# Kernel tuning notes

Hardware: AMD Instinct MI355X
Metric: run time of the kernel (lower is better)

The kernel has to match this reference:

```python
import jax, jax.numpy as jnp
import numpy as np


def conv2d(x, w, b, pad):
    # NCHW conv, stride 1, symmetric padding
    out = jax.lax.conv_general_dilated(
        x, w, window_strides=(1, 1), padding=[(pad, pad), (pad, pad)],
        dimension_numbers=("NCHW", "OIHW", "NCHW"))
    return out + b[None, :, None, None]


def setup_inputs() -> dict:
    key = jax.random.key(0)
    ks = jax.random.split(key, 18)
    B, C, H, W = 4, 256, 64, 64
    Cq = C // 16  # 16
    Ck = C // 8   # 32
    s = 0.02
    return {
        "x": jax.random.normal(ks[0], (B, C, H, W), jnp.float32),
        "dw1_w": jax.random.normal(ks[1], (Cq, C, 7, 7), jnp.float32) * s,
        "dw1_b": jnp.zeros((Cq,), jnp.float32),
        "dw2_w": jax.random.normal(ks[2], (Cq, C, 11, 11), jnp.float32) * s,
        "dw2_b": jnp.zeros((Cq,), jnp.float32),
        "key_w": jax.random.normal(ks[3], (Ck, C, 1, 1), jnp.float32) * s,
        "key_b": jnp.zeros((Ck,), jnp.float32),
        "value_w": jax.random.normal(ks[4], (C, C, 1, 1), jnp.float32) * s,
        "value_b": jnp.zeros((C,), jnp.float32),
        "conv1_w": jax.random.normal(ks[5], (Cq, C, 3, 3), jnp.float32) * s,
        "conv1_b": jnp.zeros((Cq,), jnp.float32),
        "conv2_w": jax.random.normal(ks[6], (C, Cq, 3, 3), jnp.float32) * s,
        "conv2_b": jnp.zeros((C,), jnp.float32),
        "se_w": jax.random.normal(ks[7], (C, C, 1, 1), jnp.float32) * s,
        "se_b": jnp.zeros((C,), jnp.float32),
        "gamma1": jnp.zeros((1,), jnp.float32) + 0.1,  # nonzero so attention path is exercised
        "gamma2": jnp.zeros((1,), jnp.float32) + 0.1,
    }


def reference(x, dw1_w, dw1_b, dw2_w, dw2_b, key_w, key_b, value_w, value_b,
              conv1_w, conv1_b, conv2_w, conv2_b, se_w, se_b, gamma1, gamma2):
    B, C, H, W = x.shape
    HW = H * W
    # q: concat of 7x7 and 11x11 conv branches -> (B, HW, C//8)
    q = jnp.concatenate([conv2d(x, dw1_w, dw1_b, 3), conv2d(x, dw2_w, dw2_b, 5)], axis=1)
    q = q.reshape(B, -1, HW).transpose(0, 2, 1)
    # k: 1x1 conv -> (B, C//8, HW)
    k = conv2d(x, key_w, key_b, 0).reshape(B, -1, HW)
    # raw (unscaled) full spatial attention, softmax over last dim
    att = jax.nn.softmax(jnp.einsum("bnc,bcm->bnm", q, k), axis=-1)  # (B, HW, HW)
    v = conv2d(x, value_w, value_b, 0).reshape(B, C, HW)
    out = jnp.einsum("bcm,bnm->bcn", v, att).reshape(B, C, H, W)
    # local conv branch + channel attention (SE)
    y = conv2d(jax.nn.silu(conv2d(x, conv1_w, conv1_b, 1)), conv2_w, conv2_b, 1)
    pooled = jnp.mean(y, axis=(2, 3), keepdims=True)  # (B, C, 1, 1)
    se = y * jax.nn.sigmoid(conv2d(pooled, se_w, se_b, 0))
    return gamma1 * out + gamma2 * se + x
```

## Files before the change

kernel.cpp:

```cpp
#include <hip/hip_runtime.h>

typedef unsigned short u16;
typedef unsigned u32;
typedef __bf16 bf16x8 __attribute__((ext_vector_type(8)));
typedef float f32x4 __attribute__((ext_vector_type(4)));
typedef float f32x16 __attribute__((ext_vector_type(16)));

#define MFMA16(A,B,C) __builtin_amdgcn_mfma_f32_16x16x32_bf16((A),(B),(C),0,0,0)
#define MFMA32(A,B,C) __builtin_amdgcn_mfma_f32_32x32x16_bf16((A),(B),(C),0,0,0)

__device__ __forceinline__ u16 f2b(float f){
  union { float f; unsigned u; } X; X.f = f;
  unsigned r = X.u + 0x7FFFu + ((X.u >> 16) & 1u);
  return (u16)(r >> 16);
}
__device__ __forceinline__ float b2f(u16 h){
  union { unsigned u; float f; } X; X.u = ((unsigned)h) << 16; return X.f;
}
__device__ __forceinline__ bf16x8 ld_frag(const u16* p){
  union { uint4 u; bf16x8 v; } U; U.u = *(const uint4*)p; return U.v;
}
__device__ __forceinline__ u32 pkbf(float a, float b){
  u32 r; asm("v_cvt_pk_bf16_f32 %0, %1, %2" : "=v"(r) : "v"(a), "v"(b)); return r;
}
__device__ __forceinline__ void pl32swap(u32& x, u32& y){
  auto r = __builtin_amdgcn_permlane32_swap(x, y, false, false);
  x = r[0]; y = r[1];
}
__device__ __forceinline__ void gld16(const u16* g, u16* l){
  __builtin_amdgcn_global_load_lds(
      (const __attribute__((address_space(1))) u32*)g,
      (__attribute__((address_space(3))) u32*)l, 16, 0, 0);
}

__device__ __forceinline__ void prep_w_body(int i,
    const float* __restrict__ dw1, const float* __restrict__ dw2,
    const float* __restrict__ cw1, const float* __restrict__ kw,
    const float* __restrict__ vw,  const float* __restrict__ cw2,
    u16* __restrict__ wB, u16* __restrict__ wC,
    u16* __restrict__ kwt, u16* __restrict__ vwt, u16* __restrict__ w2t,
    float* __restrict__ pooled){
  const int NB = 991232, NC = 73728, NK = 8192, NV = 65536, N2 = 40960;
  if(i < NB){
    int tap = i >> 13, rem = i & 8191;
    int chunk = rem >> 9, r2 = rem & 511;
    int oc = r2 >> 4, ci = chunk*16 + (r2 & 15);
    int dy = tap / 11, dx = tap - dy*11;
    float v;
    if(oc < 16){
      v = (dy >= 2 && dy <= 8 && dx >= 2 && dx <= 8) ? dw1[(oc*256 + ci)*49 + (dy-2)*7 + (dx-2)] : 0.f;
    } else {
      v = dw2[((oc-16)*256 + ci)*121 + tap];
    }
    wB[i] = f2b(v);
    return;
  }
  i -= NB;
  if(i < NC){
    int tap = i >> 13, rem = i & 8191;
    int chunk = rem >> 9, r2 = rem & 511;
    int oc = r2 >> 4, ci = chunk*16 + (r2 & 15);
    wC[i] = (oc < 16) ? f2b(cw1[(oc*256 + ci)*9 + tap]) : (u16)0;
    return;
  }
  i -= NC;
  if(i < NK){ kwt[i] = f2b(kw[i]); return; }
  i -= NK;
  if(i < NV){ vwt[i] = f2b(vw[i]); return; }
  i -= NV;
  if(i < N2){
    int co = i/160, kk = i - co*160;
    int tap = kk >> 4, ci = kk & 15;
    w2t[i] = (tap < 9) ? f2b(cw2[co*144 + ci*9 + tap]) : (u16)0;
    return;
  }
  i -= N2;
  if(i < 1024){ pooled[i] = 0.f; return; }
}

__device__ __forceinline__ void prep_x_body(int bid, int t, float* tile ,
    const float* __restrict__ x, u16* __restrict__ xp){
  const int b = bid >> 10, rem = bid & 1023;
  const int c0 = (rem >> 7) << 5, m0 = (rem & 127) << 5;
  { const int cg = t >> 5, mm = t & 31;
    #pragma unroll
    for(int i=0;i<4;i++)
      tile[(cg*4+i)*33 + mm] = x[((size_t)(b*256 + c0 + cg*4 + i) << 12) + m0 + mm];
  }
  __syncthreads();
  { const int cp = (t & 15) << 1, mloc = t >> 4;
    #pragma unroll
    for(int half = 0; half < 2; ++half){
      const int ml = half*16 + mloc;
      const int m = m0 + ml;
      const int yy = (m >> 6) + 5, xx = (m & 63) + 5;
      const int ci = c0 + cp;
      const int chunk = ci >> 4, wi = ci & 15;
      u16 lo = f2b(tile[cp*33 + ml]), hi = f2b(tile[(cp+1)*33 + ml]);
      *(unsigned*)&xp[(((size_t)(b*16 + chunk)*74 + yy)*80 + xx)*16 + wi] = ((unsigned)hi << 16) | lo;
    }
  }
}

__global__ __launch_bounds__(256) void k_prep(
    const float* __restrict__ x, u16* __restrict__ xp,
    const float* __restrict__ dw1, const float* __restrict__ dw2,
    const float* __restrict__ cw1, const float* __restrict__ kw,
    const float* __restrict__ vw,  const float* __restrict__ cw2,
    u16* __restrict__ wB, u16* __restrict__ wC,
    u16* __restrict__ kwt, u16* __restrict__ vwt, u16* __restrict__ w2t,
    float* __restrict__ pooled){
  __shared__ float tile[32*33];
  const int bid = blockIdx.x;
  if(bid < 4096){
    prep_x_body(bid, threadIdx.x, tile, x, xp);
  } else {
    prep_w_body((bid - 4096)*256 + threadIdx.x, dw1, dw2, cw1, kw, vw, cw2, wB, wC, kwt, vwt, w2t, pooled);
  }
}

__device__ __forceinline__ void qconv_body(int bid, int t, u16* buf ,
    const u16* __restrict__ xp, const u16* __restrict__ wB, const u16* __restrict__ wC,
    u16* __restrict__ qp){
  const int rg = bid & 15, b = (bid >> 4) & 3, kq = bid >> 6;
  const int y0 = rg << 2;
  const int wv = t >> 6, lane = t & 63;
  const int m = lane & 31, kh = lane >> 5;
  const int laneoff = m*16 + kh*8;
  const f32x16 z16 = {0.f,0.f,0.f,0.f,0.f,0.f,0.f,0.f,0.f,0.f,0.f,0.f,0.f,0.f,0.f,0.f};
  f32x16 accA = z16, accB = z16, acc1A = z16, acc1B = z16;

  #pragma unroll 1
  for(int c = 0; c < 2; ++c){
    const int chunk = kq*2 + c;
    const uint4* src = (const uint4*)(xp + ((size_t)((b*16 + chunk)*74 + y0))*1280);
    __syncthreads();
    for(int e = t; e < 2240; e += 256){
      ((uint4*)buf)[(e & 1)*1120 + (e >> 1)] = src[e];
    }
    __syncthreads();
    const u16* wBc = wB + chunk*512 + laneoff;
    const u16* wCc = wC + chunk*512 + laneoff;
    const u16* ap = buf + kh*8960 + (wv*80 + m)*8;
    bf16x8 Brow[2][11];
    #pragma unroll
    for(int dx = 0; dx < 11; ++dx) Brow[0][dx] = ld_frag(wBc + dx*8192);
    #pragma unroll
    for(int dy = 0; dy < 11; ++dy){
      if(dy < 10){
        const u16* wnext = wBc + (dy+1)*11*8192;
        #pragma unroll
        for(int dx = 0; dx < 11; ++dx) Brow[(dy+1)&1][dx] = ld_frag(wnext + dx*8192);
      }
      const u16* rowp = ap + dy*640;
      #pragma unroll
      for(int dx = 0; dx < 11; ++dx){
        bf16x8 B = Brow[dy&1][dx];
        bf16x8 A0 = ld_frag(rowp + dx*8);
        bf16x8 A1 = ld_frag(rowp + dx*8 + 256);
        accA = MFMA32(A0, B, accA);
        accB = MFMA32(A1, B, accB);
        if(dy >= 4 && dy <= 6 && dx >= 4 && dx <= 6){
          bf16x8 B1 = ld_frag(wCc + ((dy-4)*3 + (dx-4))*8192);
          acc1A = MFMA32(A0, B1, acc1A);
          acc1B = MFMA32(A1, B1, acc1B);
        }
      }
    }
  }

  u16* qb = qp + ((size_t)kq*16384 + (b << 12) + (y0 + wv)*64) * 48;
  #pragma unroll
  for(int reg = 0; reg < 16; ++reg){
    const int row = (reg & 3) + ((reg >> 2) << 3) + (kh << 2);
    qb[row*48 + m] = f2b(accA[reg]);
    qb[(32 + row)*48 + m] = f2b(accB[reg]);
    if(m < 16){
      qb[row*48 + 32 + m] = f2b(acc1A[reg]);
      qb[(32 + row)*48 + 32 + m] = f2b(acc1B[reg]);
    }
  }
}

__device__ __forceinline__ void kv_body(int bid, int tid,
    const u16* __restrict__ xp, const u16* __restrict__ vwt, const u16* __restrict__ kwt,
    const float* __restrict__ vb, const float* __restrict__ kb,
    u16* __restrict__ vt, u16* __restrict__ k_t){
  const int h = bid & 3, blk = (bid >> 2) & 63, b = bid >> 8;
  const int wv = tid >> 6, lane = tid & 63;
  const int col = lane & 15, quad = lane >> 4;
  const int m0 = (blk << 6) + (wv << 4);
  f32x4 z = {0.f,0.f,0.f,0.f};
  f32x4 av[4], ak[2];
  #pragma unroll
  for(int i=0;i<4;i++) av[i] = z;
  ak[0] = z; ak[1] = z;
  const int m = m0 + col;
  const int py = (m >> 6) + 5, pxx = (m & 63) + 5;
  #pragma unroll 1
  for(int ch = 0; ch < 8; ++ch){
    const int cio = ch*32 + quad*8;
    const int chunk = cio >> 4, wi = cio & 15;
    bf16x8 xf = ld_frag(xp + (((size_t)(b*16 + chunk)*74 + py)*80 + pxx)*16 + wi);
    #pragma unroll
    for(int ct2 = 0; ct2 < 4; ++ct2){
      bf16x8 wf = ld_frag(vwt + (((h*4 + ct2)*16 + col) << 8) + cio);
      av[ct2] = MFMA16(wf, xf, av[ct2]);
    }
    if(h == 0){
      #pragma unroll
      for(int kt = 0; kt < 2; ++kt){
        bf16x8 kf = ld_frag(kwt + ((kt*16 + col) << 8) + cio);
        ak[kt] = MFMA16(xf, kf, ak[kt]);
      }
    }
  }
  const size_t kgb = ((size_t)(b*256 + (m0 >> 4)));
  const int hi2 = col >> 3, j = col & 7;
  #pragma unroll
  for(int ct2 = 0; ct2 < 4; ++ct2){
    #pragma unroll
    for(int r = 0; r < 4; ++r){
      const int c = (h*4 + ct2)*16 + quad*4 + r;
      vt[((((kgb*8 + (c >> 5))*2 + hi2)*32) + (c & 31))*8 + j] = f2b(av[ct2][r] + vb[c]);
    }
  }
  if(h == 0){
    #pragma unroll
    for(int kt = 0; kt < 2; ++kt){
      #pragma unroll
      for(int r = 0; r < 4; ++r){
        const int mq = b*4096 + m0 + quad*4 + r;
        k_t[mq*32 + kt*16 + col] = f2b((ak[kt][r] + kb[kt*16 + col]) );
      }
    }
  }
}

__global__ __launch_bounds__(256, 2) void k_qconv_kv(
    const u16* __restrict__ xp, const u16* __restrict__ wB, const u16* __restrict__ wC,
    u16* __restrict__ qp,
    const u16* __restrict__ vwt, const u16* __restrict__ kwt,
    const float* __restrict__ vb, const float* __restrict__ kb,
    u16* __restrict__ vt, u16* __restrict__ k_t){
  __shared__ __align__(16) u16 buf[17920];
  const int bid = blockIdx.x;
  if(bid < 512) qconv_body(bid, threadIdx.x, buf, xp, wB, wC, qp);
  else          kv_body(bid - 512, threadIdx.x, xp, vwt, kwt, vb, kb, vt, k_t);
}

__global__ __launch_bounds__(256) void k_qfin(
    const u16* __restrict__ qp, const float* __restrict__ b7,
    const float* __restrict__ b11, const float* __restrict__ b1,
    u16* __restrict__ q_t, u16* __restrict__ t1){
  const int t = threadIdx.x, wv = t >> 6, lane = t & 63;
  const int px = blockIdx.x*4 + wv;
  if(lane >= 48) return;
  const size_t off = (size_t)px*48 + lane;
  float s = 0.f;
  #pragma unroll
  for(int sp = 0; sp < 8; ++sp) s += b2f(qp[off + (size_t)sp*786432]);
  const float LOG2E = 1.44269504f;
  if(lane < 16){
    q_t[px*32 + lane] = f2b((s + b7[lane]) * LOG2E);
  } else if(lane < 32){
    q_t[px*32 + lane] = f2b((s + b11[lane - 16]) * LOG2E);
  } else {
    float v = s + b1[lane - 32];
    t1[px*16 + lane - 32] = f2b(v / (1.f + __expf(-v)));
  }
}

__device__ __forceinline__ void attn_body(int bid, int t, u16* Vs ,
    const u16* __restrict__ q_t, const u16* __restrict__ k_t,
    const u16* __restrict__ vt, u16* __restrict__ Op,
    float* __restrict__ lsav){
  const int q0 = (bid & 31) << 7, b = (bid >> 5) & 3, ks = bid >> 7;
  const int wv = t >> 6, lane = t & 63;
  const int cq = lane & 31, hi = lane >> 5;

  const u16* qrow = q_t + ((size_t)(b*4096 + q0 + wv*32 + cq) << 5) + hi*8;
  const bf16x8 qf0 = ld_frag(qrow), qf1 = ld_frag(qrow + 16);
  const u16* kbase = k_t + ((size_t)(b*4096 + ks*1024 + cq) << 5) + hi*8;
  const u16* vsrc = vt + ((size_t)(b*256 + ks*64) << 12);

  const f32x16 z16 = {0.f,0.f,0.f,0.f,0.f,0.f,0.f,0.f,0.f,0.f,0.f,0.f,0.f,0.f,0.f,0.f};
  f32x16 acc[8];
  #pragma unroll
  for(int i=0;i<8;i++) acc[i] = z16;
  float lp0=0.f, lp1=0.f, lp2=0.f, lp3=0.f;

  #pragma unroll
  for(int s = 0; s < 8; ++s)
    gld16(vsrc + (size_t)(s*256 + t)*8, Vs + (s*256 + (wv << 6))*8);
  __builtin_amdgcn_sched_barrier(0);
  bf16x8 kc0 = ld_frag(kbase),        kc1 = ld_frag(kbase + 16);
  bf16x8 kc2 = ld_frag(kbase + 1024), kc3 = ld_frag(kbase + 1040);

  #pragma unroll 1
  for(int it = 0; it < 16; ++it){
    const int cur = it & 1;
    asm volatile("s_waitcnt vmcnt(4)" ::: "memory");
    __builtin_amdgcn_s_barrier();
    __builtin_amdgcn_sched_barrier(0);
    const bf16x8 ka0 = kc0, ka1 = kc1, ka2 = kc2, ka3 = kc3;
    if(it < 15){
      const u16* gb = vsrc + ((size_t)(it + 1) << 14);
      #pragma unroll
      for(int s = 0; s < 8; ++s)
        gld16(gb + (size_t)(s*256 + t)*8, Vs + (cur ^ 1)*16384 + (s*256 + (wv << 6))*8);
      __builtin_amdgcn_sched_barrier(0);
      const u16* kpn = kbase + ((size_t)(it + 1) << 11);
      kc0 = ld_frag(kpn);        kc1 = ld_frag(kpn + 16);
      kc2 = ld_frag(kpn + 1024); kc3 = ld_frag(kpn + 1040);
    }
    const u16* Vb = Vs + cur*16384 + hi*256 + cq*8;
    #pragma unroll
    for(int sub = 0; sub < 2; ++sub){
      const bf16x8 kf0 = sub ? ka2 : ka0;
      const bf16x8 kf1 = sub ? ka3 : ka1;
      f32x16 S = MFMA32(kf0, qf0, z16);
      S = MFMA32(kf1, qf1, S);
      float p[16];
      #pragma unroll
      for(int rr = 0; rr < 16; ++rr) p[rr] = exp2f(S[rr]);
      #pragma unroll
      for(int rr = 0; rr < 16; rr += 4){
        lp0 += p[rr]; lp1 += p[rr+1]; lp2 += p[rr+2]; lp3 += p[rr+3];
      }
      u32 a0 = pkbf(p[0], p[1]),   b0 = pkbf(p[4], p[5]);
      u32 a1 = pkbf(p[2], p[3]),   b1 = pkbf(p[6], p[7]);
      u32 c0 = pkbf(p[8], p[9]),   d0 = pkbf(p[12], p[13]);
      u32 c1 = pkbf(p[10], p[11]), d1 = pkbf(p[14], p[15]);
      pl32swap(a0, b0); pl32swap(a1, b1); pl32swap(c0, d0); pl32swap(c1, d1);
      union { u32 w[4]; bf16x8 v; } A0, A1;
      A0.w[0] = a0; A0.w[1] = a1; A0.w[2] = b0; A0.w[3] = b1;
      A1.w[0] = c0; A1.w[1] = c1; A1.w[2] = d0; A1.w[3] = d1;
      const u16* f0 = Vb + sub*8192;
      #pragma unroll
      for(int ct = 0; ct < 8; ++ct){
        acc[ct] = MFMA32(A0.v, ld_frag(f0 + ct*512),        acc[ct]);
        acc[ct] = MFMA32(A1.v, ld_frag(f0 + 4096 + ct*512), acc[ct]);
      }
    }
  }

  float lt = lp0 + lp1 + lp2 + lp3;
  lt += __shfl_xor(lt, 32);
  if(lane < 32)
    lsav[ks*16384 + b*4096 + q0 + wv*32 + cq] = lt;
  const float invl = 1.f / lt;
  u16* ob = Op + (((size_t)(ks*16384 + b*4096 + q0 + wv*32)) << 8) + cq;
  #pragma unroll
  for(int reg = 0; reg < 16; ++reg){
    const int row = (reg & 3) + ((reg >> 2) << 3) + (hi << 2);
    const float inv = __shfl(invl, row);
    u16* orow = ob + ((size_t)row << 8);
    #pragma unroll
    for(int ct = 0; ct < 8; ++ct)
      orow[ct*32] = f2b(acc[ct][reg] * inv);
  }
}

__device__ __forceinline__ void conv2_body(int bid, int t, u16* im_s , float* pool_s ,
    const u16* __restrict__ t1, const u16* __restrict__ w2t, const float* __restrict__ b2,
    u16* __restrict__ y_t, float* __restrict__ pooled){
  const int h = bid & 3, y = (bid >> 2) & 63, b = bid >> 8;
  if(t < 64) pool_s[t] = 0.f;
  const u16* t1b = t1 + ((size_t)(b*4096) << 4);
  { const int px = t >> 2, ci0 = (t & 3) << 2;
    #pragma unroll
    for(int tap = 0; tap < 9; ++tap){
      const int ky = (tap*11) >> 5, kx = tap - ky*3;
      const int ryy = y + ky - 1, rxx = px + kx - 1;
      uint2 val = make_uint2(0u, 0u);
      if((unsigned)ryy < 64u && (unsigned)rxx < 64u)
        val = *(const uint2*)(t1b + (((ryy << 6) + rxx) << 4) + ci0);
      *(uint2*)(im_s + px*168 + tap*16 + ci0) = val;
    }
    for(int e = t; e < 1024; e += 256){ im_s[(e >> 4)*168 + 144 + (e & 15)] = 0; }
  }
  __syncthreads();
  const int wv = t >> 6, lane = t & 63, col = lane & 15, quad = lane >> 4;
  const f32x4 z = {0.f,0.f,0.f,0.f};
  f32x4 acc[4];
  #pragma unroll
  for(int i=0;i<4;i++) acc[i] = z;
  #pragma unroll
  for(int ch = 0; ch < 5; ++ch){
    bf16x8 af = ld_frag(im_s + (wv*16 + col)*168 + ch*32 + quad*8);
    #pragma unroll
    for(int j = 0; j < 4; ++j){
      bf16x8 wf = ld_frag(w2t + ((h*4 + j)*16 + col)*160 + ch*32 + quad*8);
      acc[j] = MFMA16(af, wf, acc[j]);
    }
  }
  const int m0 = (y << 6) + (wv << 4) + (quad << 2);
  #pragma unroll
  for(int j = 0; j < 4; ++j){
    const int c = (h*4 + j)*16 + col;
    const float bias = b2[c];
    float s = 0.f;
    #pragma unroll
    for(int r = 0; r < 4; ++r){
      float v = acc[j][r] + bias;
      y_t[((size_t)(b*4096 + m0 + r) << 8) + c] = f2b(v);
      s += v;
    }
    s += __shfl_xor(s, 16); s += __shfl_xor(s, 32);
    if(quad == 0) atomicAdd(&pool_s[c - h*64], s);
  }
  __syncthreads();
  if(t < 64) atomicAdd(&pooled[b*256 + h*64 + t], pool_s[t]);
}

__global__ __launch_bounds__(256, 2) void k_attn_conv2(
    const u16* __restrict__ q_t, const u16* __restrict__ k_t,
    const u16* __restrict__ vt, u16* __restrict__ Op, float* __restrict__ lsav,
    const u16* __restrict__ t1, const u16* __restrict__ w2t, const float* __restrict__ b2,
    u16* __restrict__ y_t, float* __restrict__ pooled){
  __shared__ __align__(16) u16 shm[32768];
  const int bid = blockIdx.x;
  if(bid < 512) attn_body(bid, threadIdx.x, shm, q_t, k_t, vt, Op, lsav);
  else          conv2_body(bid - 512, threadIdx.x, shm, (float*)(shm + 10752), t1, w2t, b2, y_t, pooled);
}

__global__ __launch_bounds__(256) void k_final(
    const u16* __restrict__ Op, const u16* __restrict__ y_t, const float* __restrict__ x,
    const float* __restrict__ lsav, const float* __restrict__ pooled,
    const float* __restrict__ sew, const float* __restrict__ seb,
    const float* __restrict__ g1p, const float* __restrict__ g2p,
    float* __restrict__ out){
  __shared__ float tO[32][65];
  __shared__ float tY[32][65];
  __shared__ float gate_l[32];
  const int bid = blockIdx.x;
  const int b = bid >> 9, rem = bid & 511;
  const int c0 = (rem >> 6) << 5, m0 = (rem & 63) << 6;
  const int t = threadIdx.x;
  const float g1 = g1p[0], g2 = g2p[0];
  { const int cl = t >> 3, k0 = (t & 7) << 5;
    const int c = c0 + cl;
    const float* wr = sew + (size_t)c*256 + k0;
    const float* pr = pooled + b*256 + k0;
    float part = 0.f;
    #pragma unroll
    for(int j = 0; j < 32; j += 4){
      float4 w4 = *(const float4*)(wr + j);
      float4 p4 = *(const float4*)(pr + j);
      part += w4.x*p4.x + w4.y*p4.y + w4.z*p4.z + w4.w*p4.w;
    }
    part += __shfl_xor(part, 1); part += __shfl_xor(part, 2); part += __shfl_xor(part, 4);
    if((t & 7) == 0){
      float a = part * (1.f/4096.f) + seb[c];
      gate_l[cl] = g2 / (1.f + __expf(-a));
    }
  }
  { const int ml = t >> 2, cg = (t & 3) << 3;
    const int gq = b*4096 + m0 + ml;
    const float l0 = lsav[gq], l1 = lsav[16384 + gq], l2 = lsav[32768 + gq], l3 = lsav[49152 + gq];
    const float inv = 1.f / (l0 + l1 + l2 + l3);
    const float w0 = l0*inv, w1 = l1*inv, w2 = l2*inv, w3 = l3*inv;
    const size_t base = ((size_t)gq << 8) + c0 + cg;
    union { uint4 u; u16 s[8]; } A0, A1, A2, A3;
    A0.u = *(const uint4*)(Op + base);
    A1.u = *(const uint4*)(Op + base + ((size_t)16384 << 8));
    A2.u = *(const uint4*)(Op + base + ((size_t)32768 << 8));
    A3.u = *(const uint4*)(Op + base + ((size_t)49152 << 8));
    #pragma unroll
    for(int i = 0; i < 8; ++i)
      tO[cg+i][ml] = w0*b2f(A0.s[i]) + w1*b2f(A1.s[i]) + w2*b2f(A2.s[i]) + w3*b2f(A3.s[i]);
    const u16* yrow = y_t + base;
    uint4 yu = *(const uint4*)yrow;
    tY[cg+0][ml]=b2f((u16)(yu.x & 0xffffu)); tY[cg+1][ml]=b2f((u16)(yu.x >> 16));
    tY[cg+2][ml]=b2f((u16)(yu.y & 0xffffu)); tY[cg+3][ml]=b2f((u16)(yu.y >> 16));
    tY[cg+4][ml]=b2f((u16)(yu.z & 0xffffu)); tY[cg+5][ml]=b2f((u16)(yu.z >> 16));
    tY[cg+6][ml]=b2f((u16)(yu.w & 0xffffu)); tY[cg+7][ml]=b2f((u16)(yu.w >> 16));
  }
  __syncthreads();
  { const int cl = t >> 3, mg = (t & 7) << 3;
    const int c = c0 + cl;
    const float gate = gate_l[cl];
    const float* xrow = x + ((size_t)(b*256 + c) << 12) + m0 + mg;
    float* orow = out + ((size_t)(b*256 + c) << 12) + m0 + mg;
    float4 x0 = *(const float4*)xrow, x1 = *(const float4*)(xrow + 4);
    float4 r0, r1;
    r0.x = g1*tO[cl][mg+0] + gate*tY[cl][mg+0] + x0.x;
    r0.y = g1*tO[cl][mg+1] + gate*tY[cl][mg+1] + x0.y;
    r0.z = g1*tO[cl][mg+2] + gate*tY[cl][mg+2] + x0.z;
    r0.w = g1*tO[cl][mg+3] + gate*tY[cl][mg+3] + x0.w;
    r1.x = g1*tO[cl][mg+4] + gate*tY[cl][mg+4] + x1.x;
    r1.y = g1*tO[cl][mg+5] + gate*tY[cl][mg+5] + x1.y;
    r1.z = g1*tO[cl][mg+6] + gate*tY[cl][mg+6] + x1.z;
    r1.w = g1*tO[cl][mg+7] + gate*tY[cl][mg+7] + x1.w;
    *(float4*)orow = r0;
    *(float4*)(orow + 4) = r1;
  }
}

extern "C" void kernel_launch(void* const* d_in, const int* in_sizes, int n_in,
                              void* d_out, int out_size, void* d_ws, size_t ws_size,
                              hipStream_t stream){
  (void)in_sizes; (void)n_in; (void)out_size; (void)ws_size;
  const float* x    = (const float*)d_in[0];
  const float* dw1w = (const float*)d_in[1];
  const float* dw1b = (const float*)d_in[2];
  const float* dw2w = (const float*)d_in[3];
  const float* dw2b = (const float*)d_in[4];
  const float* keyw = (const float*)d_in[5];
  const float* keyb = (const float*)d_in[6];
  const float* valw = (const float*)d_in[7];
  const float* valb = (const float*)d_in[8];
  const float* c1w  = (const float*)d_in[9];
  const float* c1b  = (const float*)d_in[10];
  const float* c2w  = (const float*)d_in[11];
  const float* c2b  = (const float*)d_in[12];
  const float* sew  = (const float*)d_in[13];
  const float* seb  = (const float*)d_in[14];
  const float* g1   = (const float*)d_in[15];
  const float* g2   = (const float*)d_in[16];
  float* out = (float*)d_out;

  char* w = (char*)d_ws;
  auto take = [&](size_t bytes) -> char* {
    char* p = w; w += (bytes + 255) & ~(size_t)255; return p;
  };
  u16*  Op   = (u16*)  take(33554432);
  u16*  q_t  = (u16*)  take(1048576);
  u16*  k_t  = (u16*)  take(1048576);
  u16*  vt   = (u16*)  take(8388608);
  u16*  t1   = (u16*)  take(524288);
  u16*  y_t  = (u16*)  take(8388608);
  u16*  kwt  = (u16*)  take(16384);
  u16*  vwt  = (u16*)  take(131072);
  u16*  w2t  = (u16*)  take(81920);
  float* pooled = (float*)take(4096);
  float* lsav   = (float*)take(262144);

  u16*  xp = Op;
  u16*  qp = Op + 6062080;
  u16*  wB = y_t;
  u16*  wC = y_t + 991232;

  hipMemsetAsync(xp, 0, 12124160, stream);
  k_prep<<<8708, 256, 0, stream>>>(x, xp, dw1w, dw2w, c1w, keyw, valw, c2w, wB, wC, kwt, vwt, w2t, pooled);
  k_qconv_kv<<<1536, 256, 0, stream>>>(xp, wB, wC, qp, vwt, kwt, valb, keyb, vt, k_t);
  k_qfin<<<4096, 256, 0, stream>>>(qp, dw1b, dw2b, c1b, q_t, t1);
  k_attn_conv2<<<1536, 256, 0, stream>>>(q_t, k_t, vt, Op, lsav, t1, w2t, c2b, y_t, pooled);
  k_final<<<2048, 256, 0, stream>>>(Op, y_t, x, lsav, pooled, sew, seb, g1, g2, out);
}
```

Measured before the change: 236.9 us.

## Halve attention key splits and zero only padding borders of xp

The attention split-K factor drops from four to two, so each attention block loops over twice as many key tiles and the final kernel merges two partials instead of four. This cuts the partial-output traffic and the merge work, at the cost of half as many attention blocks, which may underfill the GPU. The full-buffer memset of the padded input is replaced by extra prep threads that zero only the halo border cells, removing a separate memset pass.

New measurement: 235.3 us (median of 2 runs). No clear change (-0.7%).

```diff
diff --git a/kernel.cpp b/kernel.cpp
--- a/kernel.cpp
+++ b/kernel.cpp
@@ -39,7 +39,7 @@
     const float* __restrict__ vw,  const float* __restrict__ cw2,
     u16* __restrict__ wB, u16* __restrict__ wC,
     u16* __restrict__ kwt, u16* __restrict__ vwt, u16* __restrict__ w2t,
-    float* __restrict__ pooled){
+    float* __restrict__ pooled, u16* __restrict__ xp){
   const int NB = 991232, NC = 73728, NK = 8192, NV = 65536, N2 = 40960;
   if(i < NB){
     int tap = i >> 13, rem = i & 8191;
@@ -76,6 +76,20 @@
   }
   i -= N2;
   if(i < 1024){ pooled[i] = 0.f; return; }
+  i -= 1024;
+  if(i < 116736){
+    int b = i / 29184;
+    int r1 = i - b*29184;
+    int chunk = r1 / 1824;
+    int p = r1 - chunk*1824;
+    int y, x;
+    if(p < 800){ int r = p / 80; x = p - r*80; y = (r < 5) ? r : r + 64; }
+    else { int j = p - 800; int cc = j & 15; y = 5 + (j >> 4); x = (cc < 5) ? cc : cc + 64; }
+    uint4* dst = (uint4*)&xp[(((size_t)(b*16 + chunk)*74 + y)*80 + x)*16];
+    dst[0] = make_uint4(0u,0u,0u,0u);
+    dst[1] = make_uint4(0u,0u,0u,0u);
+    return;
+  }
 }
 
 __device__ __forceinline__ void prep_x_body(int bid, int t, float* tile ,
@@ -115,7 +129,7 @@
   if(bid < 4096){
     prep_x_body(bid, threadIdx.x, tile, x, xp);
   } else {
-    prep_w_body((bid - 4096)*256 + threadIdx.x, dw1, dw2, cw1, kw, vw, cw2, wB, wC, kwt, vwt, w2t, pooled);
+    prep_w_body((bid - 4096)*256 + threadIdx.x, dw1, dw2, cw1, kw, vw, cw2, wB, wC, kwt, vwt, w2t, pooled, xp);
   }
 }
 
@@ -281,8 +295,8 @@
 
   const u16* qrow = q_t + ((size_t)(b*4096 + q0 + wv*32 + cq) << 5) + hi*8;
   const bf16x8 qf0 = ld_frag(qrow), qf1 = ld_frag(qrow + 16);
-  const u16* kbase = k_t + ((size_t)(b*4096 + ks*1024 + cq) << 5) + hi*8;
-  const u16* vsrc = vt + ((size_t)(b*256 + ks*64) << 12);
+  const u16* kbase = k_t + ((size_t)(b*4096 + ks*2048 + cq) << 5) + hi*8;
+  const u16* vsrc = vt + ((size_t)(b*256 + ks*128) << 12);
 
   const f32x16 z16 = {0.f,0.f,0.f,0.f,0.f,0.f,0.f,0.f,0.f,0.f,0.f,0.f,0.f,0.f,0.f,0.f};
   f32x16 acc[8];
@@ -298,13 +312,13 @@
   bf16x8 kc2 = ld_frag(kbase + 1024), kc3 = ld_frag(kbase + 1040);
 
   #pragma unroll 1
-  for(int it = 0; it < 16; ++it){
+  for(int it = 0; it < 32; ++it){
     const int cur = it & 1;
     asm volatile("s_waitcnt vmcnt(4)" ::: "memory");
     __builtin_amdgcn_s_barrier();
     __builtin_amdgcn_sched_barrier(0);
     const bf16x8 ka0 = kc0, ka1 = kc1, ka2 = kc2, ka3 = kc3;
-    if(it < 15){
+    if(it < 31){
       const u16* gb = vsrc + ((size_t)(it + 1) << 14);
       #pragma unroll
       for(int s = 0; s < 8; ++s)
@@ -421,8 +435,8 @@
     u16* __restrict__ y_t, float* __restrict__ pooled){
   __shared__ __align__(16) u16 shm[32768];
   const int bid = blockIdx.x;
-  if(bid < 512) attn_body(bid, threadIdx.x, shm, q_t, k_t, vt, Op, lsav);
-  else          conv2_body(bid - 512, threadIdx.x, shm, (float*)(shm + 10752), t1, w2t, b2, y_t, pooled);
+  if(bid < 256) attn_body(bid, threadIdx.x, shm, q_t, k_t, vt, Op, lsav);
+  else          conv2_body(bid - 256, threadIdx.x, shm, (float*)(shm + 10752), t1, w2t, b2, y_t, pooled);
 }
 
 __global__ __launch_bounds__(256) void k_final(
@@ -458,18 +472,16 @@
   }
   { const int ml = t >> 2, cg = (t & 3) << 3;
     const int gq = b*4096 + m0 + ml;
-    const float l0 = lsav[gq], l1 = lsav[16384 + gq], l2 = lsav[32768 + gq], l3 = lsav[49152 + gq];
-    const float inv = 1.f / (l0 + l1 + l2 + l3);
-    const float w0 = l0*inv, w1 = l1*inv, w2 = l2*inv, w3 = l3*inv;
+    const float l0 = lsav[gq], l1 = lsav[16384 + gq];
+    const float inv = 1.f / (l0 + l1);
+    const float w0 = l0*inv, w1 = l1*inv;
     const size_t base = ((size_t)gq << 8) + c0 + cg;
-    union { uint4 u; u16 s[8]; } A0, A1, A2, A3;
+    union { uint4 u; u16 s[8]; } A0, A1;
     A0.u = *(const uint4*)(Op + base);
     A1.u = *(const uint4*)(Op + base + ((size_t)16384 << 8));
-    A2.u = *(const uint4*)(Op + base + ((size_t)32768 << 8));
-    A3.u = *(const uint4*)(Op + base + ((size_t)49152 << 8));
     #pragma unroll
     for(int i = 0; i < 8; ++i)
-      tO[cg+i][ml] = w0*b2f(A0.s[i]) + w1*b2f(A1.s[i]) + w2*b2f(A2.s[i]) + w3*b2f(A3.s[i]);
+      tO[cg+i][ml] = w0*b2f(A0.s[i]) + w1*b2f(A1.s[i]);
     const u16* yrow = y_t + base;
     uint4 yu = *(const uint4*)yrow;
     tY[cg+0][ml]=b2f((u16)(yu.x & 0xffffu)); tY[cg+1][ml]=b2f((u16)(yu.x >> 16));
@@ -542,10 +554,9 @@
   u16*  wB = y_t;
   u16*  wC = y_t + 991232;
 
-  hipMemsetAsync(xp, 0, 12124160, stream);
-  k_prep<<<8708, 256, 0, stream>>>(x, xp, dw1w, dw2w, c1w, keyw, valw, c2w, wB, wC, kwt, vwt, w2t, pooled);
+  k_prep<<<9164, 256, 0, stream>>>(x, xp, dw1w, dw2w, c1w, keyw, valw, c2w, wB, wC, kwt, vwt, w2t, pooled);
   k_qconv_kv<<<1536, 256, 0, stream>>>(xp, wB, wC, qp, vwt, kwt, valb, keyb, vt, k_t);
   k_qfin<<<4096, 256, 0, stream>>>(qp, dw1b, dw2b, c1b, q_t, t1);
-  k_attn_conv2<<<1536, 256, 0, stream>>>(q_t, k_t, vt, Op, lsav, t1, w2t, c2b, y_t, pooled);
+  k_attn_conv2<<<1280, 256, 0, stream>>>(q_t, k_t, vt, Op, lsav, t1, w2t, c2b, y_t, pooled);
   k_final<<<2048, 256, 0, stream>>>(Op, y_t, x, lsav, pooled, sew, seb, g1, g2, out);
 }
```
